# Kernel optimization log

Hardware: AMD Instinct MI355X
Metric: run time of the kernel (lower is better)

## Reference

```python
import jax, jax.numpy as jnp
import numpy as np

V = 100000   # num_vertices
E = 3200000  # directed edges (symmetric: both directions of E//2 undirected edges)
B = 8        # batch of meshes
C = 3        # xyz vertex features


def setup_inputs() -> dict:
    key = jax.random.key(0)
    k1, k2, k3, k4 = jax.random.split(key, 4)
    src = jax.random.randint(k1, (E // 2,), 0, V, dtype=jnp.int32)
    dst = jax.random.randint(k2, (E // 2,), 0, V, dtype=jnp.int32)
    edge_index = jnp.stack([jnp.concatenate([src, dst]),
                            jnp.concatenate([dst, src])])  # (2, E)
    features = jax.random.normal(k3, (B, V, C), dtype=jnp.float32)
    target_features = jax.random.normal(k4, (B, V, C), dtype=jnp.float32)
    return {"features": features, "target_features": target_features,
            "edge_index": edge_index}


def _sym_laplacian(edge_index, num_nodes, dtype):
    """get_laplacian(..., normalization='sym'): L = I - D^{-1/2} A D^{-1/2}.
    Returns (lap_row, lap_col, lap_weight) as edge list with self-loops appended."""
    row, col = edge_index
    ones = jnp.ones(row.shape, dtype)
    deg = jax.ops.segment_sum(ones, row, num_segments=num_nodes)
    deg_inv_sqrt = jnp.where(deg > 0, deg, 1.0) ** -0.5
    deg_inv_sqrt = jnp.where(deg > 0, deg_inv_sqrt, 0.0)
    ew = -deg_inv_sqrt[row] * deg_inv_sqrt[col]
    loop = jnp.arange(num_nodes, dtype=row.dtype)
    lap_row = jnp.concatenate([row, loop])
    lap_col = jnp.concatenate([col, loop])
    lap_w = jnp.concatenate([ew, jnp.ones((num_nodes,), dtype)])
    return lap_row, lap_col, lap_w


def _apply_laplacian(x, lap_row, lap_col, lap_w, num_nodes):
    # x: (B, V, C) -> gather on source vertex, scale, scatter_add on target vertex
    xt = jnp.swapaxes(x, 0, 1)                       # (V, B, C)
    msg = xt[lap_row] * lap_w[:, None, None]          # (E+V, B, C)
    out = jax.ops.segment_sum(msg, lap_col, num_segments=num_nodes)  # (V, B, C)
    return jnp.swapaxes(out, 0, 1)                    # (B, V, C)


def reference(features, target_features, edge_index):
    lap_row, lap_col, lap_w = _sym_laplacian(edge_index, V, features.dtype)
    lap_x = _apply_laplacian(features, lap_row, lap_col, lap_w, V)
    lap_y = _apply_laplacian(target_features, lap_row, lap_col, lap_w, V)
    # per-batch mse averaged over batch == global mean since shapes are uniform
    return jnp.mean((lap_x - lap_y) ** 2)
```

## Files before the change

kernel.cpp:

```cpp
#include <hip/hip_runtime.h>

#define C_CONST 3
#define B_CONST 8
#define BC 24
#define NCH 3
#define VP 196
#define NP 512
#define CAP 6784
#define K1_T 512
#define K1_EPT 16
#define K1_EPB (K1_T * K1_EPT)
#define PREP_T 512
#define GT 576

typedef float floatx2 __attribute__((ext_vector_type(2)));

__global__ __launch_bounds__(K1_T) void bucket_kernel(
    const int* __restrict__ row, const int* __restrict__ col, int E,
    int* __restrict__ pcount, unsigned int* __restrict__ bucket)
{
    __shared__ unsigned int sl[K1_EPB];
    __shared__ int hist[NP];
    __shared__ int offs[NP];
    __shared__ int gbase[NP];
    __shared__ int scanbuf[NP];
    int tid = threadIdx.x;
    for (int i = tid; i < NP; i += K1_T) hist[i] = 0;
    __syncthreads();

    int e0 = blockIdx.x * K1_EPB + tid * K1_EPT;
    unsigned int pk[K1_EPT];
    int pe[K1_EPT];
    int rk[K1_EPT];
    if (e0 + K1_EPT <= E) {
        int rs[K1_EPT], cs[K1_EPT];
#pragma unroll
        for (int q = 0; q < K1_EPT / 4; q++) {
            int4 rv = *(const int4*)(row + e0 + q * 4);
            int4 cv = *(const int4*)(col + e0 + q * 4);
            rs[q*4+0] = rv.x; rs[q*4+1] = rv.y; rs[q*4+2] = rv.z; rs[q*4+3] = rv.w;
            cs[q*4+0] = cv.x; cs[q*4+1] = cv.y; cs[q*4+2] = cv.z; cs[q*4+3] = cv.w;
        }
#pragma unroll
        for (int i = 0; i < K1_EPT; i++) {
            int c = cs[i];
            int p = c / VP;
            pe[i] = p;
            pk[i] = (unsigned int)rs[i] | ((unsigned int)(c - p * VP) << 17);
        }
    } else {
#pragma unroll
        for (int i = 0; i < K1_EPT; i++) {
            int e = e0 + i;
            if (e < E) {
                int c = col[e];
                int p = c / VP;
                pe[i] = p;
                pk[i] = (unsigned int)row[e] | ((unsigned int)(c - p * VP) << 17);
            } else { pe[i] = -1; pk[i] = 0; }
        }
    }
#pragma unroll
    for (int i = 0; i < K1_EPT; i++)
        rk[i] = (pe[i] >= 0) ? atomicAdd(&hist[pe[i]], 1) : 0;
    __syncthreads();

    scanbuf[tid] = hist[tid];
    __syncthreads();
    for (int off = 1; off < NP; off <<= 1) {
        int t2 = (tid >= off) ? scanbuf[tid - off] : 0;
        __syncthreads();
        scanbuf[tid] += t2;
        __syncthreads();
    }
    offs[tid] = scanbuf[tid] - hist[tid];
    gbase[tid] = (hist[tid] > 0) ? atomicAdd(&pcount[tid], hist[tid]) : 0;
    __syncthreads();

#pragma unroll
    for (int i = 0; i < K1_EPT; i++)
        if (pe[i] >= 0) sl[offs[pe[i]] + rk[i]] = pk[i];
    __syncthreads();

    int wid = tid >> 6, lane = tid & 63;
    for (int pp = wid; pp < NP; pp += K1_T / 64) {
        int cnt = hist[pp];
        int lo = offs[pp];
        int gb = gbase[pp];
        unsigned int* dst = bucket + (size_t)pp * CAP;
        for (int i = lane; i < cnt; i += 64) {
            int pos = gb + i;
            if (pos < CAP) dst[pos] = sl[lo + i];
        }
    }
}

__global__ __launch_bounds__(PREP_T) void prep_sort_kernel(
    const int* __restrict__ pcount, unsigned int* __restrict__ bucket,
    const float* __restrict__ x, const float* __restrict__ y, int V,
    int* __restrict__ rowptr_g, unsigned char* __restrict__ wh)
{
    __shared__ unsigned int sorted[CAP];
    __shared__ int rowptr[VP + 1];
    __shared__ int cur[VP];
    __shared__ int scanbuf[256];
    __shared__ float ssc[VP];
    __shared__ unsigned char tile[VP * BC];
    int p = blockIdx.x;
    int tid = threadIdx.x;
    int n = pcount[p]; if (n > CAP) n = CAP;
    unsigned int* bp = bucket + (size_t)p * CAP;

    for (int i = tid; i < VP; i += PREP_T) cur[i] = 0;
    __syncthreads();
    for (int i = tid; i < n; i += PREP_T) atomicAdd(&cur[bp[i] >> 17], 1);
    __syncthreads();

    if (tid < 256) scanbuf[tid] = (tid < VP) ? cur[tid] : 0;
    __syncthreads();
    for (int off = 1; off < 256; off <<= 1) {
        int t2 = 0;
        if (tid < 256 && tid >= off) t2 = scanbuf[tid - off];
        __syncthreads();
        if (tid < 256) scanbuf[tid] += t2;
        __syncthreads();
    }
    if (tid == 0) rowptr[0] = 0;
    if (tid < VP) rowptr[tid + 1] = scanbuf[tid];
    for (int i = tid; i < VP; i += PREP_T) cur[i] = 0;
    __syncthreads();

    for (int i = tid; i < n; i += PREP_T) {
        unsigned int e = bp[i];
        int cl = e >> 17;
        int slot = rowptr[cl] + atomicAdd(&cur[cl], 1);
        sorted[slot] = e & 0x1FFFFu;
    }
    __syncthreads();

    for (int i = tid; i < n; i += PREP_T) bp[i] = sorted[i];
    for (int i = tid; i <= VP; i += PREP_T) rowptr_g[p * (VP + 1) + i] = rowptr[i];

    int vb = p * VP;
    int nv = V - vb; if (nv > VP) nv = VP; if (nv < 0) nv = 0;
    for (int i = tid; i < nv; i += PREP_T) {
        int dg = rowptr[i + 1] - rowptr[i];
        ssc[i] = (dg > 0) ? rsqrtf((float)dg) : 1.0f;
    }
    __syncthreads();

    int ns = nv * C_CONST;
    int ns4 = ns >> 2;
    for (int idx = tid; idx < B_CONST * ns4; idx += PREP_T) {
        int b = idx / ns4;
        int q = idx - b * ns4;
        size_t off = ((size_t)b * V + vb) * C_CONST + (size_t)q * 4;
        float4 xv = *(const float4*)(x + off);
        float4 yv = *(const float4*)(y + off);
        float vals[4] = {xv.x - yv.x, xv.y - yv.y, xv.z - yv.z, xv.w - yv.w};
        int f0 = q * 4;
#pragma unroll
        for (int j = 0; j < 4; j++) {
            int f = f0 + j;
            int vl = f / C_CONST;
            int c = f - vl * C_CONST;
            float w = ssc[vl] * vals[j];
            int packed = __builtin_amdgcn_cvt_pk_fp8_f32(w, w, 0, false);
            tile[vl * BC + b * C_CONST + c] = (unsigned char)(packed & 0xFF);
        }
    }
    __syncthreads();

    int nbytes = nv * BC;
    uint4* dst = (uint4*)(wh + (size_t)vb * BC);
    const uint4* srcT = (const uint4*)tile;
    for (int i = tid; i < (nbytes >> 4); i += PREP_T) dst[i] = srcT[i];
}

__global__ __launch_bounds__(GT) void gather_loss_kernel(
    const int* __restrict__ pcount, const unsigned int* __restrict__ sortedg,
    const int* __restrict__ rowptr_g, const uint2* __restrict__ whp,
    int V, float inv_n, float* __restrict__ out)
{
    __shared__ unsigned int sorted[CAP];
    __shared__ int rowptr[VP + 1];
    __shared__ float ls[GT / 64];
    int p = blockIdx.x;
    int tid = threadIdx.x;
    int n = pcount[p]; if (n > CAP) n = CAP;
    const unsigned int* bp = sortedg + (size_t)p * CAP;

    for (int i = tid; i < n; i += GT) sorted[i] = bp[i];
    for (int i = tid; i <= VP; i += GT) rowptr[i] = rowptr_g[p * (VP + 1) + i];
    __syncthreads();

    float s = 0.0f;
    for (int item = tid; item < VP * NCH; item += GT) {
        int cl = item / NCH;
        int j = item - cl * NCH;
        int v = p * VP + cl;
        if (v < V) {
            int q0 = rowptr[cl], q1 = rowptr[cl + 1];
            int dg = q1 - q0;
            float a0=0.f,a1=0.f,a2=0.f,a3=0.f,a4=0.f,a5=0.f,a6=0.f,a7=0.f;
            for (int q = q0; q < q1; q++) {
                int r = (int)sorted[q];
                uint2 u = whp[r * NCH + j];
                floatx2 f0 = __builtin_amdgcn_cvt_pk_f32_fp8((int)u.x, false);
                floatx2 f1 = __builtin_amdgcn_cvt_pk_f32_fp8((int)u.x, true);
                floatx2 f2 = __builtin_amdgcn_cvt_pk_f32_fp8((int)u.y, false);
                floatx2 f3 = __builtin_amdgcn_cvt_pk_f32_fp8((int)u.y, true);
                a0 += f0.x; a1 += f0.y; a2 += f1.x; a3 += f1.y;
                a4 += f2.x; a5 += f2.y; a6 += f3.x; a7 += f3.y;
            }
            float dvv = (dg > 0) ? rsqrtf((float)dg) : 0.0f;
            float di  = (dg > 0) ? sqrtf((float)dg)  : 1.0f;
            uint2 su = whp[v * NCH + j];
            floatx2 s0 = __builtin_amdgcn_cvt_pk_f32_fp8((int)su.x, false);
            floatx2 s1 = __builtin_amdgcn_cvt_pk_f32_fp8((int)su.x, true);
            floatx2 s2 = __builtin_amdgcn_cvt_pk_f32_fp8((int)su.y, false);
            floatx2 s3 = __builtin_amdgcn_cvt_pk_f32_fp8((int)su.y, true);
            float r0 = s0.x * di - dvv * a0;
            float r1 = s0.y * di - dvv * a1;
            float r2 = s1.x * di - dvv * a2;
            float r3 = s1.y * di - dvv * a3;
            float r4 = s2.x * di - dvv * a4;
            float r5 = s2.y * di - dvv * a5;
            float r6 = s3.x * di - dvv * a6;
            float r7 = s3.y * di - dvv * a7;
            s += r0*r0 + r1*r1 + r2*r2 + r3*r3 + r4*r4 + r5*r5 + r6*r6 + r7*r7;
        }
    }

    for (int off = 32; off > 0; off >>= 1) s += __shfl_down(s, off, 64);
    int lane = tid & 63;
    int wid = tid >> 6;
    if (lane == 0) ls[wid] = s;
    __syncthreads();
    if (tid == 0) {
        float tot = 0.0f;
        for (int i = 0; i < GT / 64; i++) tot += ls[i];
        atomicAdd(out, tot * inv_n);
    }
}

extern "C" void kernel_launch(void* const* d_in, const int* in_sizes, int n_in,
                              void* d_out, int out_size, void* d_ws, size_t ws_size,
                              hipStream_t stream) {
    const float* x = (const float*)d_in[0];
    const float* y = (const float*)d_in[1];
    const int*  ei = (const int*)d_in[2];

    const int E = in_sizes[2] / 2;
    const int V = in_sizes[0] / (B_CONST * C_CONST);
    const int* row = ei;
    const int* col = ei + E;

    char* ws = (char*)d_ws;
    size_t off = 0;
    unsigned int* bucket = (unsigned int*)(ws + off); off += (size_t)NP * CAP * 4;
    unsigned char* wh = (unsigned char*)(ws + off);   off += (size_t)NP * VP * BC;
    int* rowptr_g = (int*)(ws + off);  off += (size_t)NP * (VP + 1) * 4;
    int* pcount   = (int*)(ws + off);  off += (size_t)NP * 4;
    float* outf = (float*)d_out;

    hipMemsetAsync(pcount, 0, (size_t)NP * sizeof(int), stream);
    hipMemsetAsync(d_out, 0, sizeof(float), stream);

    bucket_kernel<<<(E + K1_EPB - 1) / K1_EPB, K1_T, 0, stream>>>(row, col, E, pcount, bucket);
    prep_sort_kernel<<<NP, PREP_T, 0, stream>>>(pcount, bucket, x, y, V, rowptr_g, wh);
    gather_loss_kernel<<<NP, GT, 0, stream>>>(pcount, bucket, rowptr_g,
                                              (const uint2*)wh, V,
                                              1.0f / (float)(V * BC), outf);
}
```

Measured before the change: 151.8 us.

## Replace per-partition counting sort with LDS atomic accumulation in gather

Drops the in-block counting sort and row-pointer build from the prep kernel; prep now only computes per-vertex degree counts and writes them out. The gather kernel walks the unsorted bucket edge list directly and accumulates the gathered fp8 features into a padded shared-memory accumulator with float atomics, then computes the loss per vertex. This removes the scan, scatter and bucket rewrite and balances work per edge instead of per vertex. In exchange it adds eight LDS float atomics per edge-item, which can contend, and summation order becomes nondeterministic.

New measurement: 506.9 us. 234% more time.

```diff
diff --git a/kernel.cpp b/kernel.cpp
--- a/kernel.cpp
+++ b/kernel.cpp
@@ -7,11 +7,12 @@
 #define VP 196
 #define NP 512
 #define CAP 6784
+#define ASTRIDE 25
 #define K1_T 512
 #define K1_EPT 16
 #define K1_EPB (K1_T * K1_EPT)
 #define PREP_T 512
-#define GT 576
+#define GT 512
 
 typedef float floatx2 __attribute__((ext_vector_type(2)));
 
@@ -95,56 +96,29 @@
     }
 }
 
-__global__ __launch_bounds__(PREP_T) void prep_sort_kernel(
-    const int* __restrict__ pcount, unsigned int* __restrict__ bucket,
+__global__ __launch_bounds__(PREP_T) void prep_kernel(
+    const int* __restrict__ pcount, const unsigned int* __restrict__ bucket,
     const float* __restrict__ x, const float* __restrict__ y, int V,
-    int* __restrict__ rowptr_g, unsigned char* __restrict__ wh)
+    int* __restrict__ degs, unsigned char* __restrict__ wh)
 {
-    __shared__ unsigned int sorted[CAP];
-    __shared__ int rowptr[VP + 1];
-    __shared__ int cur[VP];
-    __shared__ int scanbuf[256];
+    __shared__ int cnt[VP];
     __shared__ float ssc[VP];
     __shared__ unsigned char tile[VP * BC];
     int p = blockIdx.x;
     int tid = threadIdx.x;
     int n = pcount[p]; if (n > CAP) n = CAP;
-    unsigned int* bp = bucket + (size_t)p * CAP;
-
-    for (int i = tid; i < VP; i += PREP_T) cur[i] = 0;
-    __syncthreads();
-    for (int i = tid; i < n; i += PREP_T) atomicAdd(&cur[bp[i] >> 17], 1);
-    __syncthreads();
-
-    if (tid < 256) scanbuf[tid] = (tid < VP) ? cur[tid] : 0;
-    __syncthreads();
-    for (int off = 1; off < 256; off <<= 1) {
-        int t2 = 0;
-        if (tid < 256 && tid >= off) t2 = scanbuf[tid - off];
-        __syncthreads();
-        if (tid < 256) scanbuf[tid] += t2;
-        __syncthreads();
-    }
-    if (tid == 0) rowptr[0] = 0;
-    if (tid < VP) rowptr[tid + 1] = scanbuf[tid];
-    for (int i = tid; i < VP; i += PREP_T) cur[i] = 0;
-    __syncthreads();
-
-    for (int i = tid; i < n; i += PREP_T) {
-        unsigned int e = bp[i];
-        int cl = e >> 17;
-        int slot = rowptr[cl] + atomicAdd(&cur[cl], 1);
-        sorted[slot] = e & 0x1FFFFu;
-    }
-    __syncthreads();
-
-    for (int i = tid; i < n; i += PREP_T) bp[i] = sorted[i];
-    for (int i = tid; i <= VP; i += PREP_T) rowptr_g[p * (VP + 1) + i] = rowptr[i];
+    const unsigned int* bp = bucket + (size_t)p * CAP;
+
+    for (int i = tid; i < VP; i += PREP_T) cnt[i] = 0;
+    __syncthreads();
+    for (int i = tid; i < n; i += PREP_T) atomicAdd(&cnt[bp[i] >> 17], 1);
+    __syncthreads();
 
     int vb = p * VP;
     int nv = V - vb; if (nv > VP) nv = VP; if (nv < 0) nv = 0;
     for (int i = tid; i < nv; i += PREP_T) {
-        int dg = rowptr[i + 1] - rowptr[i];
+        int dg = cnt[i];
+        degs[vb + i] = dg;
         ssc[i] = (dg > 0) ? rsqrtf((float)dg) : 1.0f;
     }
     __syncthreads();
@@ -178,58 +152,69 @@
 }
 
 __global__ __launch_bounds__(GT) void gather_loss_kernel(
-    const int* __restrict__ pcount, const unsigned int* __restrict__ sortedg,
-    const int* __restrict__ rowptr_g, const uint2* __restrict__ whp,
+    const int* __restrict__ pcount, const unsigned int* __restrict__ bucket,
+    const int* __restrict__ degs, const uint2* __restrict__ whp,
     int V, float inv_n, float* __restrict__ out)
 {
-    __shared__ unsigned int sorted[CAP];
-    __shared__ int rowptr[VP + 1];
+    __shared__ float acc[VP * ASTRIDE];
     __shared__ float ls[GT / 64];
     int p = blockIdx.x;
     int tid = threadIdx.x;
     int n = pcount[p]; if (n > CAP) n = CAP;
-    const unsigned int* bp = sortedg + (size_t)p * CAP;
-
-    for (int i = tid; i < n; i += GT) sorted[i] = bp[i];
-    for (int i = tid; i <= VP; i += GT) rowptr[i] = rowptr_g[p * (VP + 1) + i];
-    __syncthreads();
-
+    const unsigned int* bp = bucket + (size_t)p * CAP;
+
+    for (int i = tid; i < VP * ASTRIDE; i += GT) acc[i] = 0.0f;
+    __syncthreads();
+
+    int nitems = 3 * n;
+    for (int item = tid; item < nitems; item += GT) {
+        int i = item / 3;
+        int j = item - i * 3;
+        unsigned int e = bp[i];
+        int cl = (int)(e >> 17);
+        int r  = (int)(e & 0x1FFFFu);
+        uint2 u = whp[r * NCH + j];
+        floatx2 f0 = __builtin_amdgcn_cvt_pk_f32_fp8((int)u.x, false);
+        floatx2 f1 = __builtin_amdgcn_cvt_pk_f32_fp8((int)u.x, true);
+        floatx2 f2 = __builtin_amdgcn_cvt_pk_f32_fp8((int)u.y, false);
+        floatx2 f3 = __builtin_amdgcn_cvt_pk_f32_fp8((int)u.y, true);
+        float* arow = &acc[cl * ASTRIDE + j * 8];
+        atomicAdd(&arow[0], f0.x);
+        atomicAdd(&arow[1], f0.y);
+        atomicAdd(&arow[2], f1.x);
+        atomicAdd(&arow[3], f1.y);
+        atomicAdd(&arow[4], f2.x);
+        atomicAdd(&arow[5], f2.y);
+        atomicAdd(&arow[6], f3.x);
+        atomicAdd(&arow[7], f3.y);
+    }
+    __syncthreads();
+
+    int vb = p * VP;
+    int nv = V - vb; if (nv > VP) nv = VP; if (nv < 0) nv = 0;
     float s = 0.0f;
-    for (int item = tid; item < VP * NCH; item += GT) {
-        int cl = item / NCH;
-        int j = item - cl * NCH;
-        int v = p * VP + cl;
-        if (v < V) {
-            int q0 = rowptr[cl], q1 = rowptr[cl + 1];
-            int dg = q1 - q0;
-            float a0=0.f,a1=0.f,a2=0.f,a3=0.f,a4=0.f,a5=0.f,a6=0.f,a7=0.f;
-            for (int q = q0; q < q1; q++) {
-                int r = (int)sorted[q];
-                uint2 u = whp[r * NCH + j];
-                floatx2 f0 = __builtin_amdgcn_cvt_pk_f32_fp8((int)u.x, false);
-                floatx2 f1 = __builtin_amdgcn_cvt_pk_f32_fp8((int)u.x, true);
-                floatx2 f2 = __builtin_amdgcn_cvt_pk_f32_fp8((int)u.y, false);
-                floatx2 f3 = __builtin_amdgcn_cvt_pk_f32_fp8((int)u.y, true);
-                a0 += f0.x; a1 += f0.y; a2 += f1.x; a3 += f1.y;
-                a4 += f2.x; a5 += f2.y; a6 += f3.x; a7 += f3.y;
-            }
-            float dvv = (dg > 0) ? rsqrtf((float)dg) : 0.0f;
-            float di  = (dg > 0) ? sqrtf((float)dg)  : 1.0f;
-            uint2 su = whp[v * NCH + j];
-            floatx2 s0 = __builtin_amdgcn_cvt_pk_f32_fp8((int)su.x, false);
-            floatx2 s1 = __builtin_amdgcn_cvt_pk_f32_fp8((int)su.x, true);
-            floatx2 s2 = __builtin_amdgcn_cvt_pk_f32_fp8((int)su.y, false);
-            floatx2 s3 = __builtin_amdgcn_cvt_pk_f32_fp8((int)su.y, true);
-            float r0 = s0.x * di - dvv * a0;
-            float r1 = s0.y * di - dvv * a1;
-            float r2 = s1.x * di - dvv * a2;
-            float r3 = s1.y * di - dvv * a3;
-            float r4 = s2.x * di - dvv * a4;
-            float r5 = s2.y * di - dvv * a5;
-            float r6 = s3.x * di - dvv * a6;
-            float r7 = s3.y * di - dvv * a7;
-            s += r0*r0 + r1*r1 + r2*r2 + r3*r3 + r4*r4 + r5*r5 + r6*r6 + r7*r7;
-        }
+    for (int item = tid; item < nv * NCH; item += GT) {
+        int vl = item / 3;
+        int j = item - vl * 3;
+        int v = vb + vl;
+        int dg = degs[v];
+        float dvv = (dg > 0) ? rsqrtf((float)dg) : 0.0f;
+        float di  = (dg > 0) ? sqrtf((float)dg)  : 1.0f;
+        uint2 su = whp[v * NCH + j];
+        floatx2 s0 = __builtin_amdgcn_cvt_pk_f32_fp8((int)su.x, false);
+        floatx2 s1 = __builtin_amdgcn_cvt_pk_f32_fp8((int)su.x, true);
+        floatx2 s2 = __builtin_amdgcn_cvt_pk_f32_fp8((int)su.y, false);
+        floatx2 s3 = __builtin_amdgcn_cvt_pk_f32_fp8((int)su.y, true);
+        const float* arow = &acc[vl * ASTRIDE + j * 8];
+        float r0 = s0.x * di - dvv * arow[0];
+        float r1 = s0.y * di - dvv * arow[1];
+        float r2 = s1.x * di - dvv * arow[2];
+        float r3 = s1.y * di - dvv * arow[3];
+        float r4 = s2.x * di - dvv * arow[4];
+        float r5 = s2.y * di - dvv * arow[5];
+        float r6 = s3.x * di - dvv * arow[6];
+        float r7 = s3.y * di - dvv * arow[7];
+        s += r0*r0 + r1*r1 + r2*r2 + r3*r3 + r4*r4 + r5*r5 + r6*r6 + r7*r7;
     }
 
     for (int off = 32; off > 0; off >>= 1) s += __shfl_down(s, off, 64);
@@ -260,16 +245,16 @@
     size_t off = 0;
     unsigned int* bucket = (unsigned int*)(ws + off); off += (size_t)NP * CAP * 4;
     unsigned char* wh = (unsigned char*)(ws + off);   off += (size_t)NP * VP * BC;
-    int* rowptr_g = (int*)(ws + off);  off += (size_t)NP * (VP + 1) * 4;
-    int* pcount   = (int*)(ws + off);  off += (size_t)NP * 4;
+    int* degs   = (int*)(ws + off);  off += (size_t)(NP * VP) * 4;
+    int* pcount = (int*)(ws + off);  off += (size_t)NP * 4;
     float* outf = (float*)d_out;
 
     hipMemsetAsync(pcount, 0, (size_t)NP * sizeof(int), stream);
     hipMemsetAsync(d_out, 0, sizeof(float), stream);
 
     bucket_kernel<<<(E + K1_EPB - 1) / K1_EPB, K1_T, 0, stream>>>(row, col, E, pcount, bucket);
-    prep_sort_kernel<<<NP, PREP_T, 0, stream>>>(pcount, bucket, x, y, V, rowptr_g, wh);
-    gather_loss_kernel<<<NP, GT, 0, stream>>>(pcount, bucket, rowptr_g,
+    prep_kernel<<<NP, PREP_T, 0, stream>>>(pcount, bucket, x, y, V, degs, wh);
+    gather_loss_kernel<<<NP, GT, 0, stream>>>(pcount, bucket, degs,
                                               (const uint2*)wh, V,
                                               1.0f / (float)(V * BC), outf);
 }
```
